# Performance work log

Measured on AMD Instinct MI355X. Metric: run time of the kernel, lower is better.

The kernel has to match this reference:

```python
import jax, jax.numpy as jnp
import numpy as np

N, IN_C, OUT_C = 4096, 256, 64
ALPHA = 0.2  # LeakyReLU negative slope


def setup_inputs() -> dict:
    key = jax.random.key(0)
    k1, k2, k3, k4 = jax.random.split(key, 4)
    H = jax.random.normal(k1, (N, IN_C), dtype=jnp.float32)
    adj = jax.random.randint(k2, (N, N), 0, 2, dtype=jnp.int32)
    # xavier_uniform with gain=1.414
    gain = 1.414
    limW = gain * np.sqrt(6.0 / (IN_C + OUT_C))
    W = jax.random.uniform(k3, (IN_C, OUT_C), minval=-limW, maxval=limW, dtype=jnp.float32)
    lima = gain * np.sqrt(6.0 / (2 * OUT_C + 1))
    a = jax.random.uniform(k4, (2 * OUT_C, 1), minval=-lima, maxval=lima, dtype=jnp.float32)
    return {"H": H, "adj": adj, "W": W, "a": a}


def reference(H, adj, W, a):
    Wh = H @ W  # [N, out_C]
    # Attention_Mat[i,j] = concat(Wh_i, Wh_j); score = Attention_Mat @ a
    # = (Wh @ a1)_i + (Wh @ a2)_j  -- fused, avoids the O(N^2 * 2F) tensor.
    a1, a2 = a[:OUT_C, 0], a[OUT_C:, 0]
    e = (Wh @ a1)[:, None] + (Wh @ a2)[None, :]  # [N, N]
    e = jnp.where(e > 0, e, ALPHA * e)  # LeakyReLU
    att = jax.nn.softmax(e, axis=1)
    # NOTE: original masks AFTER softmax (rows are not renormalized).
    att = jnp.where(adj > 0, att, jnp.zeros_like(att))
    out = att @ Wh  # [N, out_C]
    return jax.nn.elu(out)  # concat=True
```

## Files before the change

kernel.cpp:

```cpp
#include <hip/hip_runtime.h>
#include <math.h>

static constexpr int NN   = 4096;
static constexpr int INC  = 256;
static constexpr int OUTC = 64;

typedef _Float16 half8 __attribute__((ext_vector_type(8)));
typedef float floatx4 __attribute__((ext_vector_type(4)));

__device__ __forceinline__ float lrelu(float x) {
    return fmaxf(x, 0.f) + 0.2f * fminf(x, 0.f);
}
__device__ __forceinline__ float elu1(float x) {
    return x > 0.f ? x : (__expf(x) - 1.f);
}

__global__ __launch_bounds__(256) void k_wh(const float* __restrict__ H,
                                            const float* __restrict__ W,
                                            const float* __restrict__ a,
                                            unsigned short* __restrict__ WhT,
                                            float* __restrict__ f1,
                                            float* __restrict__ f2) {
    __shared__ __align__(16) float Wl[INC * OUTC];
    __shared__ __align__(16) float Hl[16 * INC];
    __shared__ _Float16 Tl[16 * 68];
    const int t = threadIdx.x;
    const int i0 = blockIdx.x * 16;
    {
        const float4* W4 = (const float4*)W;
        float4* Wl4 = (float4*)Wl;
        #pragma unroll
        for (int u = 0; u < 16; ++u) Wl4[u * 256 + t] = W4[u * 256 + t];
        const float4* H4 = (const float4*)(H + i0 * INC);
        float4* Hl4 = (float4*)Hl;
        #pragma unroll
        for (int u = 0; u < 4; ++u) Hl4[u * 256 + t] = H4[u * 256 + t];
    }
    __syncthreads();
    const int c = t & 63;
    const int g = t >> 6;
    const float a1c = a[c];
    const float a2c = a[OUTC + c];
    float acc[4] = {0.f, 0.f, 0.f, 0.f};
    const float4* Hl4 = (const float4*)Hl;
    for (int k4 = 0; k4 < INC / 4; ++k4) {
        const float w0 = Wl[(k4 * 4 + 0) * OUTC + c];
        const float w1 = Wl[(k4 * 4 + 1) * OUTC + c];
        const float w2 = Wl[(k4 * 4 + 2) * OUTC + c];
        const float w3 = Wl[(k4 * 4 + 3) * OUTC + c];
        #pragma unroll
        for (int s = 0; s < 4; ++s) {
            const float4 h = Hl4[(g + 4 * s) * (INC / 4) + k4];
            acc[s] = fmaf(h.x, w0, fmaf(h.y, w1, fmaf(h.z, w2, fmaf(h.w, w3, acc[s]))));
        }
    }
    #pragma unroll
    for (int s = 0; s < 4; ++s) {
        const int r = g + 4 * s;
        Tl[r * 68 + c] = (_Float16)acc[s];
        float v1 = acc[s] * a1c;
        float v2 = acc[s] * a2c;
        #pragma unroll
        for (int off = 32; off; off >>= 1) {
            v1 += __shfl_xor(v1, off);
            v2 += __shfl_xor(v2, off);
        }
        if (c == 0) { f1[i0 + r] = v1; f2[i0 + r] = v2; }
    }
    __syncthreads();
    const int c2 = t >> 2;
    const int rs = (t & 3) * 4;
    ushort4 u;
    u.x = *(const unsigned short*)&Tl[(rs + 0) * 68 + c2];
    u.y = *(const unsigned short*)&Tl[(rs + 1) * 68 + c2];
    u.z = *(const unsigned short*)&Tl[(rs + 2) * 68 + c2];
    u.w = *(const unsigned short*)&Tl[(rs + 3) * 68 + c2];
    *(ushort4*)(WhT + c2 * NN + i0 + rs) = u;
}

__global__ __launch_bounds__(256) void k_max(const float* __restrict__ f2,
                                             float* __restrict__ mx) {
    __shared__ float red[4];
    const int t = threadIdx.x;
    float m = -3.4e38f;
    const float4* f24 = (const float4*)f2;
    for (int idx = t; idx < NN / 4; idx += 256) {
        const float4 v = f24[idx];
        m = fmaxf(m, fmaxf(fmaxf(v.x, v.y), fmaxf(v.z, v.w)));
    }
    #pragma unroll
    for (int off = 32; off; off >>= 1) m = fmaxf(m, __shfl_xor(m, off));
    if ((t & 63) == 0) red[t >> 6] = m;
    __syncthreads();
    if (t == 0) mx[0] = fmaxf(fmaxf(red[0], red[1]), fmaxf(red[2], red[3]));
}

__global__ __launch_bounds__(512, 4) void k_att(const int* __restrict__ adj,
                                                const _Float16* __restrict__ WhT,
                                                const float* __restrict__ f1,
                                                const float* __restrict__ f2,
                                                const float* __restrict__ mx,
                                                float* __restrict__ numP,
                                                float* __restrict__ denP) {
    __shared__ float sacc[8 * 1024];
    __shared__ float sden[8 * 16];
    const int t = threadIdx.x;
    const int w = t >> 6;
    const int l = t & 63;
    const int m = l & 15;
    const int quad = l >> 4;
    const int rb = blockIdx.x >> 1;
    const int js = blockIdx.x & 1;
    const int i0 = rb * 16;
    const float maxf2 = mx[0];
    const float f1r = f1[i0 + m];
    const float mrow = lrelu(f1r + maxf2);
    float den = 0.f;
    floatx4 acc[4] = {{0.f,0.f,0.f,0.f},{0.f,0.f,0.f,0.f},{0.f,0.f,0.f,0.f},{0.f,0.f,0.f,0.f}};
    const int jbase = js * 2048 + w * 32 + quad * 8;
    const int* adjrow = adj + (size_t)(i0 + m) * NN;

    for (int it = 0; it < 8; ++it) {
        const int j = jbase + it * 256;
        const int4 a0 = *(const int4*)(adjrow + j);
        const int4 a1 = *(const int4*)(adjrow + j + 4);
        const float4 g0 = *(const float4*)(f2 + j);
        const float4 g1 = *(const float4*)(f2 + j + 4);
        half8 af;
        {
            float p;
            p = __expf(lrelu(f1r + g0.x) - mrow); den += p; af[0] = (a0.x > 0) ? (_Float16)p : (_Float16)0.f;
            p = __expf(lrelu(f1r + g0.y) - mrow); den += p; af[1] = (a0.y > 0) ? (_Float16)p : (_Float16)0.f;
            p = __expf(lrelu(f1r + g0.z) - mrow); den += p; af[2] = (a0.z > 0) ? (_Float16)p : (_Float16)0.f;
            p = __expf(lrelu(f1r + g0.w) - mrow); den += p; af[3] = (a0.w > 0) ? (_Float16)p : (_Float16)0.f;
            p = __expf(lrelu(f1r + g1.x) - mrow); den += p; af[4] = (a1.x > 0) ? (_Float16)p : (_Float16)0.f;
            p = __expf(lrelu(f1r + g1.y) - mrow); den += p; af[5] = (a1.y > 0) ? (_Float16)p : (_Float16)0.f;
            p = __expf(lrelu(f1r + g1.z) - mrow); den += p; af[6] = (a1.z > 0) ? (_Float16)p : (_Float16)0.f;
            p = __expf(lrelu(f1r + g1.w) - mrow); den += p; af[7] = (a1.w > 0) ? (_Float16)p : (_Float16)0.f;
        }
        #pragma unroll
        for (int nt = 0; nt < 4; ++nt) {
            const half8 bf = *(const half8*)(WhT + (size_t)(nt * 16 + m) * NN + j);
            acc[nt] = __builtin_amdgcn_mfma_f32_16x16x32_f16(af, bf, acc[nt], 0, 0, 0);
        }
    }
    den += __shfl_xor(den, 16);
    den += __shfl_xor(den, 32);
    if (l < 16) sden[w * 16 + l] = den;
    #pragma unroll
    for (int nt = 0; nt < 4; ++nt)
        #pragma unroll
        for (int r = 0; r < 4; ++r)
            sacc[w * 1024 + (quad * 4 + r) * 64 + nt * 16 + m] = acc[nt][r];
    __syncthreads();
    for (int o = t; o < 1024; o += 512) {
        float s = 0.f;
        #pragma unroll
        for (int w2 = 0; w2 < 8; ++w2) s += sacc[w2 * 1024 + o];
        numP[(size_t)js * NN * 64 + i0 * 64 + o] = s;
    }
    if (t < 16) {
        float s = 0.f;
        #pragma unroll
        for (int w2 = 0; w2 < 8; ++w2) s += sden[w2 * 16 + t];
        denP[js * NN + i0 + t] = s;
    }
}

__global__ __launch_bounds__(256) void k_fin(const float* __restrict__ numP,
                                             const float* __restrict__ denP,
                                             float* __restrict__ out) {
    const int id = blockIdx.x * 256 + threadIdx.x;
    const int i = id >> 4;
    const float4* n4 = (const float4*)numP;
    const float4 v0 = n4[id];
    const float4 v1 = n4[id + NN * 16];
    const float den = denP[i] + denP[NN + i];
    const float inv = 1.f / den;
    float4 o;
    o.x = elu1((v0.x + v1.x) * inv);
    o.y = elu1((v0.y + v1.y) * inv);
    o.z = elu1((v0.z + v1.z) * inv);
    o.w = elu1((v0.w + v1.w) * inv);
    ((float4*)out)[id] = o;
}

extern "C" void kernel_launch(void* const* d_in, const int* in_sizes, int n_in,
                              void* d_out, int out_size, void* d_ws, size_t ws_size,
                              hipStream_t stream) {
    const float* H  = (const float*)d_in[0];
    const int* adj  = (const int*)d_in[1];
    const float* W  = (const float*)d_in[2];
    const float* a  = (const float*)d_in[3];
    float* out = (float*)d_out;
    char* ws = (char*)d_ws;
    unsigned short* WhT = (unsigned short*)(ws);
    float* f1   = (float*)(ws + (512 << 10));
    float* f2   = (float*)(ws + (528 << 10));
    float* mx   = (float*)(ws + (544 << 10));
    float* denP = (float*)(ws + (560 << 10));
    float* numP = (float*)(ws + (1 << 20));
    hipLaunchKernelGGL(k_wh,  dim3(256), dim3(256), 0, stream, H, W, a, WhT, f1, f2);
    hipLaunchKernelGGL(k_max, dim3(1),   dim3(256), 0, stream, f2, mx);
    hipLaunchKernelGGL(k_att, dim3(512), dim3(512), 0, stream, adj, (const _Float16*)WhT, f1, f2, mx, numP, denP);
    hipLaunchKernelGGL(k_fin, dim3(256), dim3(256), 0, stream, numP, denP, out);
}
```

Baseline: 129.9 us.

## Fuse max reduction and finalize into attention kernel with 1024-thread blocks

Drops the separate single-block max kernel and the finalize kernel. Each attention block now copies f2 into shared memory, computes the global max there, and handles a full 4096-column row strip with 16 waves instead of splitting it across two blocks. The block then reduces across waves and applies normalization and ELU directly, removing two launches and the numP/denP round trip through global memory. In exchange, every block redundantly reduces f2, uses much more shared memory, and the grid shrinks to 256 blocks, which may reduce occupancy and latency hiding on the adj stream.

```diff
diff --git a/kernel.cpp b/kernel.cpp
--- a/kernel.cpp
+++ b/kernel.cpp
@@ -78,54 +78,49 @@
     *(ushort4*)(WhT + c2 * NN + i0 + rs) = u;
 }
 
-__global__ __launch_bounds__(256) void k_max(const float* __restrict__ f2,
-                                             float* __restrict__ mx) {
-    __shared__ float red[4];
-    const int t = threadIdx.x;
-    float m = -3.4e38f;
-    const float4* f24 = (const float4*)f2;
-    for (int idx = t; idx < NN / 4; idx += 256) {
-        const float4 v = f24[idx];
-        m = fmaxf(m, fmaxf(fmaxf(v.x, v.y), fmaxf(v.z, v.w)));
-    }
-    #pragma unroll
-    for (int off = 32; off; off >>= 1) m = fmaxf(m, __shfl_xor(m, off));
-    if ((t & 63) == 0) red[t >> 6] = m;
-    __syncthreads();
-    if (t == 0) mx[0] = fmaxf(fmaxf(red[0], red[1]), fmaxf(red[2], red[3]));
-}
-
-__global__ __launch_bounds__(512, 4) void k_att(const int* __restrict__ adj,
-                                                const _Float16* __restrict__ WhT,
-                                                const float* __restrict__ f1,
-                                                const float* __restrict__ f2,
-                                                const float* __restrict__ mx,
-                                                float* __restrict__ numP,
-                                                float* __restrict__ denP) {
-    __shared__ float sacc[8 * 1024];
-    __shared__ float sden[8 * 16];
+__global__ __launch_bounds__(1024, 4) void k_att(const int* __restrict__ adj,
+                                                 const _Float16* __restrict__ WhT,
+                                                 const float* __restrict__ f1,
+                                                 const float* __restrict__ f2,
+                                                 float* __restrict__ out) {
+    __shared__ __align__(16) float sf2[NN];
+    __shared__ __align__(16) float sacc[16 * 1024];
+    __shared__ float sden[16 * 16];
+    __shared__ float smax[16];
     const int t = threadIdx.x;
     const int w = t >> 6;
     const int l = t & 63;
     const int m = l & 15;
     const int quad = l >> 4;
-    const int rb = blockIdx.x >> 1;
-    const int js = blockIdx.x & 1;
-    const int i0 = rb * 16;
-    const float maxf2 = mx[0];
+    const int i0 = blockIdx.x * 16;
+
+    {
+        const float4 v = ((const float4*)f2)[t];
+        ((float4*)sf2)[t] = v;
+        float mloc = fmaxf(fmaxf(v.x, v.y), fmaxf(v.z, v.w));
+        #pragma unroll
+        for (int off = 32; off; off >>= 1) mloc = fmaxf(mloc, __shfl_xor(mloc, off));
+        if (l == 0) smax[w] = mloc;
+    }
+    __syncthreads();
+    float maxf2 = smax[0];
+    #pragma unroll
+    for (int k = 1; k < 16; ++k) maxf2 = fmaxf(maxf2, smax[k]);
+
     const float f1r = f1[i0 + m];
     const float mrow = lrelu(f1r + maxf2);
     float den = 0.f;
     floatx4 acc[4] = {{0.f,0.f,0.f,0.f},{0.f,0.f,0.f,0.f},{0.f,0.f,0.f,0.f},{0.f,0.f,0.f,0.f}};
-    const int jbase = js * 2048 + w * 32 + quad * 8;
+    const int jbase = w * 32 + quad * 8;
     const int* adjrow = adj + (size_t)(i0 + m) * NN;
 
+    #pragma unroll 2
     for (int it = 0; it < 8; ++it) {
-        const int j = jbase + it * 256;
+        const int j = jbase + it * 512;
         const int4 a0 = *(const int4*)(adjrow + j);
         const int4 a1 = *(const int4*)(adjrow + j + 4);
-        const float4 g0 = *(const float4*)(f2 + j);
-        const float4 g1 = *(const float4*)(f2 + j + 4);
+        const float4 g0 = *(const float4*)(sf2 + j);
+        const float4 g1 = *(const float4*)(sf2 + j + 4);
         half8 af;
         {
             float p;
@@ -153,36 +148,14 @@
         for (int r = 0; r < 4; ++r)
             sacc[w * 1024 + (quad * 4 + r) * 64 + nt * 16 + m] = acc[nt][r];
     __syncthreads();
-    for (int o = t; o < 1024; o += 512) {
-        float s = 0.f;
-        #pragma unroll
-        for (int w2 = 0; w2 < 8; ++w2) s += sacc[w2 * 1024 + o];
-        numP[(size_t)js * NN * 64 + i0 * 64 + o] = s;
-    }
-    if (t < 16) {
-        float s = 0.f;
-        #pragma unroll
-        for (int w2 = 0; w2 < 8; ++w2) s += sden[w2 * 16 + t];
-        denP[js * NN + i0 + t] = s;
-    }
-}
-
-__global__ __launch_bounds__(256) void k_fin(const float* __restrict__ numP,
-                                             const float* __restrict__ denP,
-                                             float* __restrict__ out) {
-    const int id = blockIdx.x * 256 + threadIdx.x;
-    const int i = id >> 4;
-    const float4* n4 = (const float4*)numP;
-    const float4 v0 = n4[id];
-    const float4 v1 = n4[id + NN * 16];
-    const float den = denP[i] + denP[NN + i];
-    const float inv = 1.f / den;
-    float4 o;
-    o.x = elu1((v0.x + v1.x) * inv);
-    o.y = elu1((v0.y + v1.y) * inv);
-    o.z = elu1((v0.z + v1.z) * inv);
-    o.w = elu1((v0.w + v1.w) * inv);
-    ((float4*)out)[id] = o;
+    float s = 0.f;
+    #pragma unroll
+    for (int w2 = 0; w2 < 16; ++w2) s += sacc[w2 * 1024 + t];
+    float dden = 0.f;
+    const int row = t >> 6;
+    #pragma unroll
+    for (int w2 = 0; w2 < 16; ++w2) dden += sden[w2 * 16 + row];
+    out[(size_t)i0 * OUTC + t] = elu1(s / dden);
 }
 
 extern "C" void kernel_launch(void* const* d_in, const int* in_sizes, int n_in,
@@ -197,11 +170,6 @@
     unsigned short* WhT = (unsigned short*)(ws);
     float* f1   = (float*)(ws + (512 << 10));
     float* f2   = (float*)(ws + (528 << 10));
-    float* mx   = (float*)(ws + (544 << 10));
-    float* denP = (float*)(ws + (560 << 10));
-    float* numP = (float*)(ws + (1 << 20));
-    hipLaunchKernelGGL(k_wh,  dim3(256), dim3(256), 0, stream, H, W, a, WhT, f1, f2);
-    hipLaunchKernelGGL(k_max, dim3(1),   dim3(256), 0, stream, f2, mx);
-    hipLaunchKernelGGL(k_att, dim3(512), dim3(512), 0, stream, adj, (const _Float16*)WhT, f1, f2, mx, numP, denP);
-    hipLaunchKernelGGL(k_fin, dim3(256), dim3(256), 0, stream, numP, denP, out);
+    hipLaunchKernelGGL(k_wh,  dim3(256), dim3(256),  0, stream, H, W, a, WhT, f1, f2);
+    hipLaunchKernelGGL(k_att, dim3(256), dim3(1024), 0, stream, adj, (const _Float16*)WhT, f1, f2, out);
 }
```

Result: no change. 128.5 us (-1.1%).
